# Optimization experiments

Measured on AMD Instinct MI355X. Metric: run time of the kernel, lower is better.

## Reference

```python
import jax, jax.numpy as jnp
import numpy as np

UNITS, B, I, H = 8, 65536, 256, 256


def setup_inputs() -> dict:
    key = jax.random.key(0)
    k_x, k_wi, k_wh, k_bi, k_bh = jax.random.split(key, 5)
    scale = 1.0 / np.sqrt(H)  # torch GRUCell init range ~ U(-1/sqrt(H), 1/sqrt(H))
    return {
        "x": jax.random.normal(k_x, (B, I), dtype=jnp.float32),
        "W_ih": jax.random.uniform(k_wi, (UNITS, 3 * H, I), jnp.float32, -scale, scale),
        "W_hh": jax.random.uniform(k_wh, (UNITS, 3 * H, H), jnp.float32, -scale, scale),
        "b_ih": jax.random.uniform(k_bi, (UNITS, 3 * H), jnp.float32, -scale, scale),
        "b_hh": jax.random.uniform(k_bh, (UNITS, 3 * H), jnp.float32, -scale, scale),
        "h0": jnp.zeros((H,), dtype=jnp.float32),
    }


def _gru_chain(x, W_ih, W_hh, b_ih, b_hh, h0):
    # h starts as h0 broadcast over batch; each of the `units` cells consumes
    # the SAME x and the previous cell's output as hidden state.
    h_init = jnp.broadcast_to(h0, (x.shape[0], h0.shape[0]))

    def step(h, params):
        Wih, Whh, bih, bhh = params
        gi = x @ Wih.T + bih            # [B, 3H] input gates
        gh = h @ Whh.T + bhh            # [B, 3H] hidden gates
        i_r, i_z, i_n = jnp.split(gi, 3, axis=-1)  # torch gate order: r, z, n
        h_r, h_z, h_n = jnp.split(gh, 3, axis=-1)
        r = jax.nn.sigmoid(i_r + h_r)
        z = jax.nn.sigmoid(i_z + h_z)
        n = jnp.tanh(i_n + r * h_n)
        h_new = (1.0 - z) * n + z * h
        return h_new, None

    h_final, _ = jax.lax.scan(step, h_init, (W_ih, W_hh, b_ih, b_hh))
    return h_final


def reference(x, W_ih, W_hh, b_ih, b_hh, h0):
    return _gru_chain(x, W_ih, W_hh, b_ih, b_hh, h0)
```

## Files before the change

### kernel.cpp

```cpp
#include <hip/hip_runtime.h>
#include <hip/hip_bf16.h>

typedef __bf16 bf16;
typedef __bf16 bf16x4 __attribute__((ext_vector_type(4)));
typedef __bf16 bf16x8 __attribute__((ext_vector_type(8)));
typedef float f32x4 __attribute__((ext_vector_type(4)));

#define GLD16(gp, sp) __builtin_amdgcn_global_load_lds( \
    (const __attribute__((address_space(1))) void*)(gp), \
    (__attribute__((address_space(3))) void*)(sp), 16, 0, 0)

#define FENCE() asm volatile("" ::: "memory")
#define BARRIER() do { FENCE(); __builtin_amdgcn_s_barrier(); FENCE(); } while (0)

constexpr int UNITS = 8;
constexpr int BATCH = 65536;
constexpr int DIM   = 256;
constexpr int BM    = 256;
constexpr int BN    = 16;
constexpr int BK    = 64;
constexpr int JT    = DIM / BN;
constexpr int STEPS_PER_UNIT = JT * 4;
constexpr int TOT_STEPS = UNITS * STEPS_PER_UNIT;
constexpr int WTILE = 3 * BN * BK;
constexpr size_t WN = (size_t)UNITS * 3 * DIM * DIM;

__device__ __forceinline__ float sigmoidf_fast(float x) {
    return 1.0f / (1.0f + __expf(-x));
}
__device__ __forceinline__ float tanhf_fast(float x) {
    float y = fminf(fmaxf(x, -15.0f), 15.0f);
    float e = __expf(-2.0f * y);
    return (1.0f - e) / (1.0f + e);
}
__device__ __forceinline__ unsigned hsoff(int row, int col) {
    return (unsigned)((row * DIM + col) * 2) ^ (unsigned)((row & 7) << 4);
}
__device__ __forceinline__ float bfbits2f(unsigned b) {
    return __builtin_bit_cast(float, b << 16);
}
__device__ __forceinline__ unsigned f2bfbits(float f) {
    return (unsigned)__builtin_bit_cast(unsigned short, (bf16)f);
}

__global__ void convert_kernel(const float* __restrict__ Wih,
                               const float* __restrict__ Whh,
                               const float* __restrict__ bih,
                               const float* __restrict__ bhh,
                               bf16* __restrict__ Wihbf,
                               bf16* __restrict__ Whhbf,
                               float* __restrict__ bcomb)
{
    const size_t W4 = 2 * WN / 4;
    size_t i = (size_t)blockIdx.x * blockDim.x + threadIdx.x;
    if (i < W4) {
        size_t e = i * 4;
        const float* src = (e < WN) ? Wih : Whh;
        bf16* dst        = (e < WN) ? Wihbf : Whhbf;
        size_t off       = (e < WN) ? e : e - WN;
        const float4 v = *(const float4*)(src + off);
        bf16x4 o;
        o[0] = (bf16)v.x; o[1] = (bf16)v.y; o[2] = (bf16)v.z; o[3] = (bf16)v.w;
        *(bf16x4*)(dst + off) = o;
    } else {
        size_t j = i - W4;
        if (j < (size_t)UNITS * 1024) {
            int u = (int)(j >> 10), t = (int)(j & 1023);
            const float* bi = bih + u * 768;
            const float* bh = bhh + u * 768;
            float v;
            if (t < 512)      v = bi[t] + bh[t];
            else if (t < 768) v = bi[t];
            else              v = bh[t - 256];
            bcomb[u * 1024 + t] = v;
        }
    }
}

__device__ __forceinline__ void stage_w(const bf16* __restrict__ Wihbf,
                                        const bf16* __restrict__ Whhbf,
                                        bf16* wb, int sg, int wave, int lane)
{
    const int u    = sg >> 6;
    const int jt   = (sg >> 2) & 15;
    const int pair = sg & 3;
    const int k0   = pair * 64;
    const bf16* Wi = Wihbf + (size_t)u * (3 * DIM * DIM);
    const bf16* Wh = Whhbf + (size_t)u * (3 * DIM * DIM);
    const int rr   = lane >> 3;
    const int scol = ((lane & 7) ^ rr) << 3;
    {
        const int c  = wave;
        const bf16* W = (c < 6) ? Wi : Wh;
        const int cc = (c < 6) ? c : c - 6;
        bf16* d = wb + ((c < 6) ? 0 : WTILE) + cc * 512;
        const int r = cc * 8 + rr;
        const int grow = (r >> 4) * DIM + jt * BN + (r & 15);
        GLD16(W + (size_t)grow * DIM + k0 + scol, d);
    }
    if (wave < 4) {
        const int cc = wave + 2;
        const int r = cc * 8 + rr;
        const int grow = (r >> 4) * DIM + jt * BN + (r & 15);
        GLD16(Wh + (size_t)grow * DIM + k0 + scol, wb + WTILE + cc * 512);
    }
}

__global__ __launch_bounds__(512, 2)
void gru_fused_kernel(const float* __restrict__ xg,
                      const float* __restrict__ h0g,
                      const bf16* __restrict__ Wihbf,
                      const bf16* __restrict__ Whhbf,
                      const float* __restrict__ bcomb,
                      float* __restrict__ out)
{
    __shared__ __align__(16) bf16 hs[BM * DIM];
    __shared__ __align__(16) bf16 wbuf[2][2 * WTILE];

    const int tid  = threadIdx.x;
    const int wave = tid >> 6;
    const int lane = tid & 63;
    const int quad = lane >> 4;
    const int l15  = lane & 15;
    const int odd  = l15 & 1;
    const int m0   = blockIdx.x * BM;

    bf16x8 xf[2][8];
#pragma unroll
    for (int mt = 0; mt < 2; ++mt) {
        const int row = m0 + wave * 32 + mt * 16 + l15;
        const float* xr = xg + (size_t)row * DIM + quad * 8;
#pragma unroll
        for (int kc = 0; kc < 8; ++kc) {
            const float4 a = *(const float4*)(xr + kc * 32);
            const float4 b = *(const float4*)(xr + kc * 32 + 4);
            bf16x8 v;
            v[0]=(bf16)a.x; v[1]=(bf16)a.y; v[2]=(bf16)a.z; v[3]=(bf16)a.w;
            v[4]=(bf16)b.x; v[5]=(bf16)b.y; v[6]=(bf16)b.z; v[7]=(bf16)b.w;
            xf[mt][kc] = v;
        }
    }

    bf16x8 hf[2][8];
#pragma unroll
    for (int kc = 0; kc < 8; ++kc) {
        const float4 a = *(const float4*)(h0g + kc * 32 + quad * 8);
        const float4 b = *(const float4*)(h0g + kc * 32 + quad * 8 + 4);
        bf16x8 v;
        v[0]=(bf16)a.x; v[1]=(bf16)a.y; v[2]=(bf16)a.z; v[3]=(bf16)a.w;
        v[4]=(bf16)b.x; v[5]=(bf16)b.y; v[6]=(bf16)b.z; v[7]=(bf16)b.w;
        hf[0][kc] = v;
        hf[1][kc] = v;
    }
#pragma unroll
    for (int mt = 0; mt < 2; ++mt)
#pragma unroll
        for (int kc = 0; kc < 8; ++kc)
            *(bf16x8*)((char*)hs + hsoff(wave * 32 + mt * 16 + l15,
                                         kc * 32 + quad * 8)) = hf[mt][kc];

    stage_w(Wihbf, Whhbf, (bf16*)wbuf[0], 0, wave, lane);

    for (int u = 0; u < UNITS; ++u) {
        const float* bc = bcomb + u * 1024;
        for (int jt = 0; jt < JT; ++jt) {
            const int jc = jt * BN + l15;
            const float br  = bc[jc];
            const float bz  = bc[DIM + jc];
            const float bni = bc[2 * DIM + jc];
            const float bnh = bc[3 * DIM + jc];

            f32x4 acc[4][2];
#pragma unroll
            for (int g = 0; g < 4; ++g)
#pragma unroll
                for (int mt = 0; mt < 2; ++mt)
                    acc[g][mt] = (f32x4){0.f, 0.f, 0.f, 0.f};

            const int sg0 = u * STEPS_PER_UNIT + jt * 4;
#pragma unroll
            for (int pair = 0; pair < 4; ++pair) {
                const int sg = sg0 + pair;
                asm volatile("s_waitcnt vmcnt(0)" ::: "memory");
                BARRIER();
                if (sg + 1 < TOT_STEPS)
                    stage_w(Wihbf, Whhbf, (bf16*)wbuf[(sg + 1) & 1],
                            sg + 1, wave, lane);
                const bf16* wt = wbuf[sg & 1];
#pragma unroll
                for (int kc2 = 0; kc2 < 2; ++kc2) {
                    const int kcg = pair * 2 + kc2;
                    bf16x8 bi[3], bh[3];
#pragma unroll
                    for (int g = 0; g < 3; ++g) {
                        const int off = (g * BN + l15) * BK
                                      + (((kc2 * 4 + quad) ^ (l15 & 7)) << 3);
                        bi[g] = *(const bf16x8*)(wt + off);
                        bh[g] = *(const bf16x8*)(wt + WTILE + off);
                    }
#pragma unroll
                    for (int mt = 0; mt < 2; ++mt) {
                        acc[0][mt] = __builtin_amdgcn_mfma_f32_16x16x32_bf16(xf[mt][kcg], bi[0], acc[0][mt], 0, 0, 0);
                        acc[0][mt] = __builtin_amdgcn_mfma_f32_16x16x32_bf16(hf[mt][kcg], bh[0], acc[0][mt], 0, 0, 0);
                        acc[1][mt] = __builtin_amdgcn_mfma_f32_16x16x32_bf16(xf[mt][kcg], bi[1], acc[1][mt], 0, 0, 0);
                        acc[1][mt] = __builtin_amdgcn_mfma_f32_16x16x32_bf16(hf[mt][kcg], bh[1], acc[1][mt], 0, 0, 0);
                        acc[2][mt] = __builtin_amdgcn_mfma_f32_16x16x32_bf16(xf[mt][kcg], bi[2], acc[2][mt], 0, 0, 0);
                        acc[3][mt] = __builtin_amdgcn_mfma_f32_16x16x32_bf16(hf[mt][kcg], bh[2], acc[3][mt], 0, 0, 0);
                    }
                }
            }

#pragma unroll
            for (int mt = 0; mt < 2; ++mt) {
                const int rbase = wave * 32 + mt * 16 + quad * 4;
                const int rowA  = rbase + 2 * odd;
                const int colb  = jt * BN + (l15 & ~1);
                const unsigned d0 = *(const unsigned*)((const char*)hs + hsoff(rowA,     colb));
                const unsigned d1 = *(const unsigned*)((const char*)hs + hsoff(rowA + 1, colb));
                const unsigned o0 = (unsigned)__shfl_xor((int)d0, 1);
                const unsigned o1 = (unsigned)__shfl_xor((int)d1, 1);
                const unsigned p0 = odd ? o0 : d0;
                const unsigned p1 = odd ? o1 : d1;
                const unsigned p2 = odd ? d0 : o0;
                const unsigned p3 = odd ? d1 : o1;
                const int sh = odd ? 16 : 0;
                float hp[4];
                hp[0] = bfbits2f((p0 >> sh) & 0xffffu);
                hp[1] = bfbits2f((p1 >> sh) & 0xffffu);
                hp[2] = bfbits2f((p2 >> sh) & 0xffffu);
                hp[3] = bfbits2f((p3 >> sh) & 0xffffu);
                unsigned bb[4];
#pragma unroll
                for (int i = 0; i < 4; ++i) {
                    const float r_ = sigmoidf_fast(acc[0][mt][i] + br);
                    const float z_ = sigmoidf_fast(acc[1][mt][i] + bz);
                    const float n_ = tanhf_fast(acc[2][mt][i] + bni
                                                + r_ * (acc[3][mt][i] + bnh));
                    const float hv = fmaf(z_, hp[i] - n_, n_);
                    bb[i] = f2bfbits(hv);
                }
                const unsigned lo  = bb[0] | (bb[1] << 16);
                const unsigned hi  = bb[2] | (bb[3] << 16);
                const unsigned olo = (unsigned)__shfl_xor((int)lo, 1);
                const unsigned ohi = (unsigned)__shfl_xor((int)hi, 1);
                unsigned w0, w1;
                if (odd) {
                    w0 = (ohi & 0xffffu) | (hi << 16);
                    w1 = (ohi >> 16)     | (hi & 0xffff0000u);
                } else {
                    w0 = (lo & 0xffffu)  | (olo << 16);
                    w1 = (lo >> 16)      | (olo & 0xffff0000u);
                }
                *(unsigned*)((char*)hs + hsoff(rowA,     colb)) = w0;
                *(unsigned*)((char*)hs + hsoff(rowA + 1, colb)) = w1;
            }
        }
        if (u < UNITS - 1) {
#pragma unroll
            for (int mt = 0; mt < 2; ++mt)
#pragma unroll
                for (int kc = 0; kc < 8; ++kc)
                    hf[mt][kc] = *(const bf16x8*)((const char*)hs +
                        hsoff(wave * 32 + mt * 16 + l15, kc * 32 + quad * 8));
        }
    }

    __syncthreads();
    {
        const int c8 = (tid & 31) * 8;
        const int r0 = tid >> 5;
#pragma unroll
        for (int i = 0; i < 16; ++i) {
            const int r = r0 + i * 16;
            const bf16x8 v = *(const bf16x8*)((const char*)hs + hsoff(r, c8));
            float4 a, b;
            a.x = (float)v[0]; a.y = (float)v[1]; a.z = (float)v[2]; a.w = (float)v[3];
            b.x = (float)v[4]; b.y = (float)v[5]; b.z = (float)v[6]; b.w = (float)v[7];
            float* o = out + (size_t)(m0 + r) * DIM + c8;
            *(float4*)o       = a;
            *(float4*)(o + 4) = b;
        }
    }
}

extern "C" void kernel_launch(void* const* d_in, const int* in_sizes, int n_in,
                              void* d_out, int out_size, void* d_ws, size_t ws_size,
                              hipStream_t stream) {
    const float* x   = (const float*)d_in[0];
    const float* Wih = (const float*)d_in[1];
    const float* Whh = (const float*)d_in[2];
    const float* bih = (const float*)d_in[3];
    const float* bhh = (const float*)d_in[4];
    const float* h0  = (const float*)d_in[5];
    float* out = (float*)d_out;

    bf16* Wihbf  = (bf16*)d_ws;
    bf16* Whhbf  = Wihbf + WN;
    float* bcomb = (float*)(Whhbf + WN);

    {
        const size_t total = 2 * WN / 4 + (size_t)UNITS * 1024;
        const int cblocks = (int)((total + 255) / 256);
        hipLaunchKernelGGL(convert_kernel, dim3(cblocks), dim3(256), 0, stream,
                           Wih, Whh, bih, bhh, Wihbf, Whhbf, bcomb);
    }
    hipLaunchKernelGGL(gru_fused_kernel, dim3(BATCH / BM), dim3(512), 0, stream,
                       x, h0, Wihbf, Whhbf, bcomb, out);
}
```

Baseline: 708.9 us.

## Halve block rows and K-step, read weight fragments before staging next tile

Cuts the block tile from 256 to 128 rows with 256 threads and narrows the weight K-step from 64 to 32, reworking the staging swizzle and step indexing to match. Each weight tile fragment is now read from LDS before the next tile's async copy is issued, and the MFMA burst runs at raised wave priority. The smaller LDS footprint per block is meant to allow more resident blocks and better latency hiding. The cost is twice as many barriers per output tile and twice as many weight loads from L2 across the grid.

```diff
diff --git a/kernel.cpp b/kernel.cpp
--- a/kernel.cpp
+++ b/kernel.cpp
@@ -16,11 +16,12 @@
 constexpr int UNITS = 8;
 constexpr int BATCH = 65536;
 constexpr int DIM   = 256;
-constexpr int BM    = 256;
+constexpr int BM    = 128;
 constexpr int BN    = 16;
-constexpr int BK    = 64;
+constexpr int BK    = 32;
+constexpr int KC    = DIM / BK;
 constexpr int JT    = DIM / BN;
-constexpr int STEPS_PER_UNIT = JT * 4;
+constexpr int STEPS_PER_UNIT = JT * KC;
 constexpr int TOT_STEPS = UNITS * STEPS_PER_UNIT;
 constexpr int WTILE = 3 * BN * BK;
 constexpr size_t WN = (size_t)UNITS * 3 * DIM * DIM;
@@ -81,32 +82,30 @@
                                         const bf16* __restrict__ Whhbf,
                                         bf16* wb, int sg, int wave, int lane)
 {
-    const int u    = sg >> 6;
-    const int jt   = (sg >> 2) & 15;
-    const int pair = sg & 3;
-    const int k0   = pair * 64;
+    const int u  = sg >> 7;
+    const int jt = (sg >> 3) & 15;
+    const int kc = sg & 7;
+    const int k0 = kc * BK;
     const bf16* Wi = Wihbf + (size_t)u * (3 * DIM * DIM);
     const bf16* Wh = Whhbf + (size_t)u * (3 * DIM * DIM);
-    const int rr   = lane >> 3;
-    const int scol = ((lane & 7) ^ rr) << 3;
+    const int rr   = lane >> 2;
+    const int scol = ((lane & 3) ^ ((rr ^ (rr >> 2)) & 3)) << 3;
     {
-        const int c  = wave;
-        const bf16* W = (c < 6) ? Wi : Wh;
-        const int cc = (c < 6) ? c : c - 6;
-        bf16* d = wb + ((c < 6) ? 0 : WTILE) + cc * 512;
-        const int r = cc * 8 + rr;
-        const int grow = (r >> 4) * DIM + jt * BN + (r & 15);
+        const int c = wave;
+        const bf16* W = (c < 3) ? Wi : Wh;
+        const int g  = (c < 3) ? c : 0;
+        bf16* d = wb + ((c < 3) ? 0 : WTILE) + g * 512;
+        const int grow = g * DIM + jt * BN + rr;
         GLD16(W + (size_t)grow * DIM + k0 + scol, d);
     }
-    if (wave < 4) {
-        const int cc = wave + 2;
-        const int r = cc * 8 + rr;
-        const int grow = (r >> 4) * DIM + jt * BN + (r & 15);
-        GLD16(Wh + (size_t)grow * DIM + k0 + scol, wb + WTILE + cc * 512);
-    }
-}
-
-__global__ __launch_bounds__(512, 2)
+    if (wave < 2) {
+        const int g = wave + 1;
+        const int grow = g * DIM + jt * BN + rr;
+        GLD16(Wh + (size_t)grow * DIM + k0 + scol, wb + WTILE + g * 512);
+    }
+}
+
+__global__ __launch_bounds__(256, 2)
 void gru_fused_kernel(const float* __restrict__ xg,
                       const float* __restrict__ h0g,
                       const bf16* __restrict__ Wihbf,
@@ -177,37 +176,35 @@
                 for (int mt = 0; mt < 2; ++mt)
                     acc[g][mt] = (f32x4){0.f, 0.f, 0.f, 0.f};
 
-            const int sg0 = u * STEPS_PER_UNIT + jt * 4;
-#pragma unroll
-            for (int pair = 0; pair < 4; ++pair) {
-                const int sg = sg0 + pair;
+            const int sg0 = u * STEPS_PER_UNIT + jt * KC;
+#pragma unroll
+            for (int kc = 0; kc < KC; ++kc) {
+                const int sg = sg0 + kc;
                 asm volatile("s_waitcnt vmcnt(0)" ::: "memory");
                 BARRIER();
+                const bf16* wt = wbuf[sg & 1];
+                bf16x8 bi[3], bh[3];
+                const int slot = (quad ^ ((l15 ^ (l15 >> 2)) & 3)) << 3;
+#pragma unroll
+                for (int g = 0; g < 3; ++g) {
+                    const int off = (g * BN + l15) * BK + slot;
+                    bi[g] = *(const bf16x8*)(wt + off);
+                    bh[g] = *(const bf16x8*)(wt + WTILE + off);
+                }
                 if (sg + 1 < TOT_STEPS)
                     stage_w(Wihbf, Whhbf, (bf16*)wbuf[(sg + 1) & 1],
                             sg + 1, wave, lane);
-                const bf16* wt = wbuf[sg & 1];
-#pragma unroll
-                for (int kc2 = 0; kc2 < 2; ++kc2) {
-                    const int kcg = pair * 2 + kc2;
-                    bf16x8 bi[3], bh[3];
-#pragma unroll
-                    for (int g = 0; g < 3; ++g) {
-                        const int off = (g * BN + l15) * BK
-                                      + (((kc2 * 4 + quad) ^ (l15 & 7)) << 3);
-                        bi[g] = *(const bf16x8*)(wt + off);
-                        bh[g] = *(const bf16x8*)(wt + WTILE + off);
-                    }
-#pragma unroll
-                    for (int mt = 0; mt < 2; ++mt) {
-                        acc[0][mt] = __builtin_amdgcn_mfma_f32_16x16x32_bf16(xf[mt][kcg], bi[0], acc[0][mt], 0, 0, 0);
-                        acc[0][mt] = __builtin_amdgcn_mfma_f32_16x16x32_bf16(hf[mt][kcg], bh[0], acc[0][mt], 0, 0, 0);
-                        acc[1][mt] = __builtin_amdgcn_mfma_f32_16x16x32_bf16(xf[mt][kcg], bi[1], acc[1][mt], 0, 0, 0);
-                        acc[1][mt] = __builtin_amdgcn_mfma_f32_16x16x32_bf16(hf[mt][kcg], bh[1], acc[1][mt], 0, 0, 0);
-                        acc[2][mt] = __builtin_amdgcn_mfma_f32_16x16x32_bf16(xf[mt][kcg], bi[2], acc[2][mt], 0, 0, 0);
-                        acc[3][mt] = __builtin_amdgcn_mfma_f32_16x16x32_bf16(hf[mt][kcg], bh[2], acc[3][mt], 0, 0, 0);
-                    }
+                __builtin_amdgcn_s_setprio(1);
+#pragma unroll
+                for (int mt = 0; mt < 2; ++mt) {
+                    acc[0][mt] = __builtin_amdgcn_mfma_f32_16x16x32_bf16(xf[mt][kc], bi[0], acc[0][mt], 0, 0, 0);
+                    acc[0][mt] = __builtin_amdgcn_mfma_f32_16x16x32_bf16(hf[mt][kc], bh[0], acc[0][mt], 0, 0, 0);
+                    acc[1][mt] = __builtin_amdgcn_mfma_f32_16x16x32_bf16(xf[mt][kc], bi[1], acc[1][mt], 0, 0, 0);
+                    acc[1][mt] = __builtin_amdgcn_mfma_f32_16x16x32_bf16(hf[mt][kc], bh[1], acc[1][mt], 0, 0, 0);
+                    acc[2][mt] = __builtin_amdgcn_mfma_f32_16x16x32_bf16(xf[mt][kc], bi[2], acc[2][mt], 0, 0, 0);
+                    acc[3][mt] = __builtin_amdgcn_mfma_f32_16x16x32_bf16(hf[mt][kc], bh[2], acc[3][mt], 0, 0, 0);
                 }
+                __builtin_amdgcn_s_setprio(0);
             }
 
 #pragma unroll
@@ -271,7 +268,7 @@
         const int r0 = tid >> 5;
 #pragma unroll
         for (int i = 0; i < 16; ++i) {
-            const int r = r0 + i * 16;
+            const int r = r0 + i * 8;
             const bf16x8 v = *(const bf16x8*)((const char*)hs + hsoff(r, c8));
             float4 a, b;
             a.x = (float)v[0]; a.y = (float)v[1]; a.z = (float)v[2]; a.w = (float)v[3];
@@ -304,6 +301,6 @@
         hipLaunchKernelGGL(convert_kernel, dim3(cblocks), dim3(256), 0, stream,
                            Wih, Whh, bih, bhh, Wihbf, Whhbf, bcomb);
     }
-    hipLaunchKernelGGL(gru_fused_kernel, dim3(BATCH / BM), dim3(512), 0, stream,
+    hipLaunchKernelGGL(gru_fused_kernel, dim3(BATCH / BM), dim3(256), 0, stream,
                        x, h0, Wihbf, Whhbf, bcomb, out);
 }
```

Result: no change. 701.8 us (-1.0%).

## Software-pipeline LDS weight reads with MFMAs and fold biases into accumulator init

Applied to the files above, without the earlier changes.

Restructures the per-tile K loop so the second half-chunk of weight fragments is read from shared memory after the current MFMAs and consumed before the next barrier. This overlaps LDS reads with matrix work across the barrier instead of serializing read-then-compute. The combined biases are now preloaded into the accumulators and prefetched one tile ahead, which removes the bias adds and the dependent global loads from the gate epilogue. MFMA bursts are wrapped in s_setprio to favour the math waves. In exchange, register pressure rises from the double set of fragment registers, which may hurt scheduling under the 512x2 launch bound.

```diff
diff --git a/kernel.cpp b/kernel.cpp
--- a/kernel.cpp
+++ b/kernel.cpp
@@ -20,7 +20,8 @@
 constexpr int BN    = 16;
 constexpr int BK    = 64;
 constexpr int JT    = DIM / BN;
-constexpr int STEPS_PER_UNIT = JT * 4;
+constexpr int PAIRS = DIM / BK;
+constexpr int STEPS_PER_UNIT = JT * PAIRS;
 constexpr int TOT_STEPS = UNITS * STEPS_PER_UNIT;
 constexpr int WTILE = 3 * BN * BK;
 constexpr size_t WN = (size_t)UNITS * 3 * DIM * DIM;
@@ -106,6 +107,30 @@
     }
 }
 
+#define READ6(BI, BH, WT, KC2) do {                                          \
+    _Pragma("unroll")                                                        \
+    for (int g_ = 0; g_ < 3; ++g_) {                                         \
+        const int off_ = (g_ * BN + l15) * BK                                \
+                       + ((((KC2) * 4 + quad) ^ (l15 & 7)) << 3);            \
+        BI[g_] = *(const bf16x8*)((WT) + off_);                              \
+        BH[g_] = *(const bf16x8*)((WT) + WTILE + off_);                      \
+    }                                                                        \
+} while (0)
+
+#define MFMA12(BI, BH, KCG) do {                                             \
+    __builtin_amdgcn_s_setprio(1);                                           \
+    _Pragma("unroll")                                                        \
+    for (int mt_ = 0; mt_ < 2; ++mt_) {                                      \
+        acc[0][mt_] = __builtin_amdgcn_mfma_f32_16x16x32_bf16(xf[mt_][KCG], BI[0], acc[0][mt_], 0, 0, 0); \
+        acc[0][mt_] = __builtin_amdgcn_mfma_f32_16x16x32_bf16(hf[mt_][KCG], BH[0], acc[0][mt_], 0, 0, 0); \
+        acc[1][mt_] = __builtin_amdgcn_mfma_f32_16x16x32_bf16(xf[mt_][KCG], BI[1], acc[1][mt_], 0, 0, 0); \
+        acc[1][mt_] = __builtin_amdgcn_mfma_f32_16x16x32_bf16(hf[mt_][KCG], BH[1], acc[1][mt_], 0, 0, 0); \
+        acc[2][mt_] = __builtin_amdgcn_mfma_f32_16x16x32_bf16(xf[mt_][KCG], BI[2], acc[2][mt_], 0, 0, 0); \
+        acc[3][mt_] = __builtin_amdgcn_mfma_f32_16x16x32_bf16(hf[mt_][KCG], BH[2], acc[3][mt_], 0, 0, 0); \
+    }                                                                        \
+    __builtin_amdgcn_s_setprio(0);                                           \
+} while (0)
+
 __global__ __launch_bounds__(512, 2)
 void gru_fused_kernel(const float* __restrict__ xg,
                       const float* __restrict__ h0g,
@@ -159,56 +184,55 @@
             *(bf16x8*)((char*)hs + hsoff(wave * 32 + mt * 16 + l15,
                                          kc * 32 + quad * 8)) = hf[mt][kc];
 
+    float bc0, bc1, bc2, bc3;
+    float bn0 = 0.f, bn1 = 0.f, bn2 = 0.f, bn3 = 0.f;
+    {
+        const float* bp = bcomb + l15;
+        bc0 = bp[0]; bc1 = bp[256]; bc2 = bp[512]; bc3 = bp[768];
+    }
     stage_w(Wihbf, Whhbf, (bf16*)wbuf[0], 0, wave, lane);
 
     for (int u = 0; u < UNITS; ++u) {
-        const float* bc = bcomb + u * 1024;
         for (int jt = 0; jt < JT; ++jt) {
-            const int jc = jt * BN + l15;
-            const float br  = bc[jc];
-            const float bz  = bc[DIM + jc];
-            const float bni = bc[2 * DIM + jc];
-            const float bnh = bc[3 * DIM + jc];
-
             f32x4 acc[4][2];
 #pragma unroll
-            for (int g = 0; g < 4; ++g)
-#pragma unroll
-                for (int mt = 0; mt < 2; ++mt)
-                    acc[g][mt] = (f32x4){0.f, 0.f, 0.f, 0.f};
-
-            const int sg0 = u * STEPS_PER_UNIT + jt * 4;
-#pragma unroll
-            for (int pair = 0; pair < 4; ++pair) {
-                const int sg = sg0 + pair;
+            for (int mt = 0; mt < 2; ++mt) {
+                acc[0][mt] = (f32x4){bc0, bc0, bc0, bc0};
+                acc[1][mt] = (f32x4){bc1, bc1, bc1, bc1};
+                acc[2][mt] = (f32x4){bc2, bc2, bc2, bc2};
+                acc[3][mt] = (f32x4){bc3, bc3, bc3, bc3};
+            }
+            bf16x8 biA[3], bhA[3], biB[3], bhB[3];
+            const int sgb = u * STEPS_PER_UNIT + jt * PAIRS;
+
+#pragma unroll
+            for (int pair = 0; pair < PAIRS; ++pair) {
+                if (pair == 1) MFMA12(biB, bhB, 1);
+                if (pair == 2) MFMA12(biB, bhB, 3);
+                if (pair == 3) MFMA12(biB, bhB, 5);
+
                 asm volatile("s_waitcnt vmcnt(0)" ::: "memory");
                 BARRIER();
-                if (sg + 1 < TOT_STEPS)
-                    stage_w(Wihbf, Whhbf, (bf16*)wbuf[(sg + 1) & 1],
-                            sg + 1, wave, lane);
-                const bf16* wt = wbuf[sg & 1];
-#pragma unroll
-                for (int kc2 = 0; kc2 < 2; ++kc2) {
-                    const int kcg = pair * 2 + kc2;
-                    bf16x8 bi[3], bh[3];
-#pragma unroll
-                    for (int g = 0; g < 3; ++g) {
-                        const int off = (g * BN + l15) * BK
-                                      + (((kc2 * 4 + quad) ^ (l15 & 7)) << 3);
-                        bi[g] = *(const bf16x8*)(wt + off);
-                        bh[g] = *(const bf16x8*)(wt + WTILE + off);
-                    }
-#pragma unroll
-                    for (int mt = 0; mt < 2; ++mt) {
-                        acc[0][mt] = __builtin_amdgcn_mfma_f32_16x16x32_bf16(xf[mt][kcg], bi[0], acc[0][mt], 0, 0, 0);
-                        acc[0][mt] = __builtin_amdgcn_mfma_f32_16x16x32_bf16(hf[mt][kcg], bh[0], acc[0][mt], 0, 0, 0);
-                        acc[1][mt] = __builtin_amdgcn_mfma_f32_16x16x32_bf16(xf[mt][kcg], bi[1], acc[1][mt], 0, 0, 0);
-                        acc[1][mt] = __builtin_amdgcn_mfma_f32_16x16x32_bf16(hf[mt][kcg], bh[1], acc[1][mt], 0, 0, 0);
-                        acc[2][mt] = __builtin_amdgcn_mfma_f32_16x16x32_bf16(xf[mt][kcg], bi[2], acc[2][mt], 0, 0, 0);
-                        acc[3][mt] = __builtin_amdgcn_mfma_f32_16x16x32_bf16(hf[mt][kcg], bh[2], acc[3][mt], 0, 0, 0);
+                const bf16* wt = wbuf[pair & 1];
+                READ6(biA, bhA, wt, 0);
+                if (sgb + pair + 1 < TOT_STEPS)
+                    stage_w(Wihbf, Whhbf, (bf16*)wbuf[(pair + 1) & 1],
+                            sgb + pair + 1, wave, lane);
+                if (pair == 1) {
+                    const int njt = (jt + 1) & 15;
+                    const int nu  = (jt == 15) ? u + 1 : u;
+                    if (nu < UNITS) {
+                        const float* bp = bcomb + nu * 1024 + njt * BN + l15;
+                        bn0 = bp[0]; bn1 = bp[256]; bn2 = bp[512]; bn3 = bp[768];
                     }
                 }
+                if (pair == 0) MFMA12(biA, bhA, 0);
+                if (pair == 1) MFMA12(biA, bhA, 2);
+                if (pair == 2) MFMA12(biA, bhA, 4);
+                if (pair == 3) MFMA12(biA, bhA, 6);
+                READ6(biB, bhB, wt, 1);
             }
+            MFMA12(biB, bhB, 7);
 
 #pragma unroll
             for (int mt = 0; mt < 2; ++mt) {
@@ -232,10 +256,9 @@
                 unsigned bb[4];
 #pragma unroll
                 for (int i = 0; i < 4; ++i) {
-                    const float r_ = sigmoidf_fast(acc[0][mt][i] + br);
-                    const float z_ = sigmoidf_fast(acc[1][mt][i] + bz);
-                    const float n_ = tanhf_fast(acc[2][mt][i] + bni
-                                                + r_ * (acc[3][mt][i] + bnh));
+                    const float r_ = sigmoidf_fast(acc[0][mt][i]);
+                    const float z_ = sigmoidf_fast(acc[1][mt][i]);
+                    const float n_ = tanhf_fast(acc[2][mt][i] + r_ * acc[3][mt][i]);
                     const float hv = fmaf(z_, hp[i] - n_, n_);
                     bb[i] = f2bfbits(hv);
                 }
@@ -254,6 +277,7 @@
                 *(unsigned*)((char*)hs + hsoff(rowA,     colb)) = w0;
                 *(unsigned*)((char*)hs + hsoff(rowA + 1, colb)) = w1;
             }
+            bc0 = bn0; bc1 = bn1; bc2 = bn2; bc3 = bn3;
         }
         if (u < UNITS - 1) {
 #pragma unroll
```

Result: no change. 700.8 us (-1.1%).
